# Kernel optimization log

Hardware: AMD Instinct MI355X
Metric: run time of the kernel (lower is better)

The kernel has to match this reference:

```python
import jax, jax.numpy as jnp
import numpy as np

N_NODES = 100000


def gcn_layer(x, W, b, src, dst, n):
    # PyG GCNConv: h = x @ W; add self loops; norm = d^-1/2[src]*d^-1/2[dst];
    # out = scatter_add(norm * h[src] -> dst) + b
    h = x @ W  # [N, F_out]
    # append self loops
    loop = jnp.arange(n, dtype=src.dtype)
    s = jnp.concatenate([src, loop])
    d = jnp.concatenate([dst, loop])
    deg = jax.ops.segment_sum(jnp.ones_like(d, dtype=h.dtype), d, num_segments=n)
    dinv = jnp.where(deg > 0, jax.lax.rsqrt(deg), 0.0)
    norm = dinv[s] * dinv[d]  # [E+N]
    msg = h[s] * norm[:, None]  # gather + scale
    out = jax.ops.segment_sum(msg, d, num_segments=n)  # scatter-add
    return out + b


def setup_inputs() -> dict:
    key = jax.random.key(0)
    k1, k2, k3, k4 = jax.random.split(key, 4)
    din, dh = 64, 64
    x = jax.random.normal(k1, (N_NODES, din), dtype=jnp.float32)
    edge_index = jax.random.randint(k2, (2, 1600000), 0, N_NODES, dtype=jnp.int64)
    s1 = 1.0 / np.sqrt(din)
    s2 = 1.0 / np.sqrt(dh)
    W1 = jax.random.uniform(k3, (din, dh), dtype=jnp.float32, minval=-s1, maxval=s1)
    W2 = jax.random.uniform(k4, (dh, dh), dtype=jnp.float32, minval=-s2, maxval=s2)
    b1 = jnp.zeros((dh,), dtype=jnp.float32)
    b2 = jnp.zeros((dh,), dtype=jnp.float32)
    return {"x": x, "edge_index": edge_index, "W1": W1, "b1": b1, "W2": W2, "b2": b2}


def reference(x, edge_index, W1, b1, W2, b2):
    src, dst = edge_index[0], edge_index[1]
    n = x.shape[0]
    h = jax.nn.relu(gcn_layer(x, W1, b1, src, dst, n))
    h = jax.nn.relu(gcn_layer(h, W2, b2, src, dst, n))
    return h
```

## Files before the change

kernel.cpp:

```cpp
#include <hip/hip_runtime.h>
#include <hip/hip_bf16.h>

using bf16s = __hip_bfloat16;
typedef __bf16 bf16x8 __attribute__((ext_vector_type(8)));
typedef float f32x4 __attribute__((ext_vector_type(4)));

constexpr int MS_TILE = 2048;
constexpr int BSH = 7;
constexpr int BN = 128;
constexpr int NBUCK_MAX = 1024;
constexpr int SLAB_CAP = 2560;
constexpr int CSR_CAP = 3584;

__device__ inline float uasf(unsigned u) { return __uint_as_float(u); }

__device__ inline unsigned pk2(float x, float y) {
    unsigned ux = __float_as_uint(x), uy = __float_as_uint(y);
    ux = (ux + 0x7fffu + ((ux >> 16) & 1u)) >> 16;
    uy = (uy + 0x7fffu + ((uy >> 16) & 1u)) & 0xffff0000u;
    return (ux & 0xffffu) | uy;
}

__global__ __launch_bounds__(256) void multisplit(const int* __restrict__ src,
                                                  const int* __restrict__ dst,
                                                  int* __restrict__ gcur,
                                                  int* __restrict__ part, int E) {
    __shared__ int cnt[NBUCK_MAX];
    __shared__ int off[NBUCK_MAX];
    __shared__ int gbase[NBUCK_MAX];
    __shared__ int img[MS_TILE];
    __shared__ int tgt[MS_TILE];
    int tid = threadIdx.x;
    for (int tbase = blockIdx.x * MS_TILE; tbase < E; tbase += gridDim.x * MS_TILE) {
        int m = min(MS_TILE, E - tbase);
        for (int i = tid; i < NBUCK_MAX; i += 256) cnt[i] = 0;
        __syncthreads();
        int pk[8], bk[8], rk[8];
        int nloc = 0;
        int j0 = tid * 8;
        if (j0 + 8 <= m) {
            int4 s0 = *(const int4*)(src + tbase + j0);
            int4 s1 = *(const int4*)(src + tbase + j0 + 4);
            int4 d0 = *(const int4*)(dst + tbase + j0);
            int4 d1 = *(const int4*)(dst + tbase + j0 + 4);
            int ss[8] = {s0.x, s0.y, s0.z, s0.w, s1.x, s1.y, s1.z, s1.w};
            int dd[8] = {d0.x, d0.y, d0.z, d0.w, d1.x, d1.y, d1.z, d1.w};
#pragma unroll
            for (int k = 0; k < 8; k++) {
                int b = dd[k] >> BSH;
                pk[k] = (ss[k] << BSH) | (dd[k] & (BN - 1));
                bk[k] = b;
                rk[k] = atomicAdd(&cnt[b], 1);
            }
            nloc = 8;
        } else {
            for (int j = j0; j < m; j++) {
                int s = src[tbase + j], d = dst[tbase + j];
                int b = d >> BSH;
                pk[nloc] = (s << BSH) | (d & (BN - 1));
                bk[nloc] = b;
                rk[nloc] = atomicAdd(&cnt[b], 1);
                nloc++;
            }
        }
        __syncthreads();
        if (tid < 64) {
            int base = tid * 16;
            int vals[16];
            int s0 = 0;
#pragma unroll
            for (int j = 0; j < 16; j++) { vals[j] = cnt[base + j]; s0 += vals[j]; }
            int sc = s0;
#pragma unroll
            for (int o = 1; o < 64; o <<= 1) {
                int u = __shfl_up(sc, o);
                if (tid >= o) sc += u;
            }
            int ex = sc - s0;
#pragma unroll
            for (int j = 0; j < 16; j++) { off[base + j] = ex; ex += vals[j]; }
        }
        __syncthreads();
        for (int b = tid; b < NBUCK_MAX; b += 256) {
            int c = cnt[b];
            if (c) {
                int st = atomicAdd(&gcur[b], c);
                if (st > SLAB_CAP - c) st = SLAB_CAP - c;
                gbase[b] = b * SLAB_CAP + st;
            }
        }
        __syncthreads();
        for (int i = 0; i < nloc; i++) {
            int p = off[bk[i]] + rk[i];
            img[p] = pk[i];
            tgt[p] = gbase[bk[i]] + rk[i];
        }
        __syncthreads();
        for (int j = tid; j < m; j += 256) part[tgt[j]] = img[j];
        __syncthreads();
    }
}

__global__ __launch_bounds__(256) void bucket_place(const int* __restrict__ gcur,
                                                    const int* __restrict__ part,
                                                    int2* __restrict__ rinfo,
                                                    int* __restrict__ csr,
                                                    float* __restrict__ dinv, int n) {
    __shared__ int cnt[BN];
    __shared__ int cur[BN];
    __shared__ int wtot[4];
    __shared__ int img[CSR_CAP];
    int b = blockIdx.x;
    int tid = threadIdx.x;
    int node0 = b << BSH;
    int m = min(gcur[b], SLAB_CAP);
    const int* slab = part + b * SLAB_CAP;
    if (tid < BN) cnt[tid] = 0;
    __syncthreads();
    for (int j = tid; j < m; j += 256) atomicAdd(&cnt[slab[j] & (BN - 1)], 1);
    __syncthreads();
    int deg = (tid < BN) ? cnt[tid] : 0;
    int pdeg = (deg + 7) & ~7;
    int lane = tid & 63, wv = tid >> 6;
    int sc = pdeg;
#pragma unroll
    for (int o = 1; o < 64; o <<= 1) {
        int u = __shfl_up(sc, o);
        if (lane >= o) sc += u;
    }
    if (lane == 63) wtot[wv] = sc;
    __syncthreads();
    int mpad = wtot[0] + wtot[1];
    if (tid < BN) {
        int ex = sc - pdeg + (wv ? wtot[0] : 0);
        cur[tid] = ex;
        int node = node0 + tid;
        if (node < n) {
            rinfo[node] = make_int2(b * CSR_CAP + ex, pdeg);
            dinv[node] = rsqrtf((float)(deg + 1));
        }
    }
    __syncthreads();
    int sent = n << 5;
    for (int j = tid; j < mpad; j += 256) img[j] = sent;
    __syncthreads();
    for (int j = tid; j < m; j += 256) {
        int pkv = slab[j];
        int p = atomicAdd(&cur[pkv & (BN - 1)], 1);
        img[p] = (pkv >> BSH) << 5;
    }
    __syncthreads();
    int* dp = csr + b * CSR_CAP;
    for (int j = tid; j < mpad; j += 256) dp[j] = img[j];
}

template <bool AF32>
__global__ __launch_bounds__(256) void gemm64(const void* __restrict__ A_,
                                              const float* __restrict__ W,
                                              const float* __restrict__ dinv,
                                              bf16s* __restrict__ out, int nrows) {
    int lane = threadIdx.x & 63;
    int wid = (blockIdx.x * blockDim.x + threadIdx.x) >> 6;
    int nwaves = (gridDim.x * blockDim.x) >> 6;
    int r = lane & 15;
    int q = lane >> 4;
    int kb = q * 8;

    if (wid == 0) out[(size_t)nrows * 64 + lane] = __float2bfloat16(0.f);

    bf16x8 bfrag[4][2];
#pragma unroll
    for (int t = 0; t < 4; t++) {
#pragma unroll
        for (int h = 0; h < 2; h++) {
            bf16x8 bb;
            int ncol = t * 16 + r;
            int k0 = h * 32 + kb;
#pragma unroll
            for (int j = 0; j < 8; j++) bb[j] = (__bf16)W[(k0 + j) * 64 + ncol];
            bfrag[t][h] = bb;
        }
    }

    int ntiles = nrows >> 4;
    for (int tile = wid; tile < ntiles; tile += nwaves) {
        bf16x8 a0, a1;
        if (AF32) {
            const float* ap = (const float*)A_ + (size_t)(tile * 16 + r) * 64 + kb;
            f32x4 v0 = *reinterpret_cast<const f32x4*>(ap);
            f32x4 v1 = *reinterpret_cast<const f32x4*>(ap + 4);
            f32x4 v2 = *reinterpret_cast<const f32x4*>(ap + 32);
            f32x4 v3 = *reinterpret_cast<const f32x4*>(ap + 36);
#pragma unroll
            for (int j = 0; j < 4; j++) {
                a0[j] = (__bf16)v0[j]; a0[4 + j] = (__bf16)v1[j];
                a1[j] = (__bf16)v2[j]; a1[4 + j] = (__bf16)v3[j];
            }
        } else {
            const __bf16* ap = (const __bf16*)A_ + (size_t)(tile * 16 + r) * 64 + kb;
            a0 = *reinterpret_cast<const bf16x8*>(ap);
            a1 = *reinterpret_cast<const bf16x8*>(ap + 32);
        }
        f32x4 c[4];
#pragma unroll
        for (int t = 0; t < 4; t++) {
            f32x4 acc = {0.f, 0.f, 0.f, 0.f};
            acc = __builtin_amdgcn_mfma_f32_16x16x32_bf16(a0, bfrag[t][0], acc, 0, 0, 0);
            acc = __builtin_amdgcn_mfma_f32_16x16x32_bf16(a1, bfrag[t][1], acc, 0, 0, 0);
            c[t] = acc;
        }
        float dr[4];
#pragma unroll
        for (int g = 0; g < 4; g++) dr[g] = dinv[tile * 16 + q * 4 + g];
#pragma unroll
        for (int t = 0; t < 4; t++) {
#pragma unroll
            for (int g = 0; g < 4; g++) {
                int row = tile * 16 + q * 4 + g;
                out[(size_t)row * 64 + t * 16 + r] = __float2bfloat16(c[t][g] * dr[g]);
            }
        }
    }
}

template <bool OUTF32>
__global__ __launch_bounds__(256) void aggregate(const unsigned* __restrict__ t32,
                                                 const float* __restrict__ dinv,
                                                 const int2* __restrict__ rinfo,
                                                 const int* __restrict__ csr,
                                                 const float* __restrict__ bias,
                                                 void* __restrict__ out_, int n) {
    int gid = blockIdx.x * blockDim.x + threadIdx.x;
    int v = gid >> 4;
    if (v >= n) return;
    int c = gid & 15;
    int2 ri = rinfo[v];
    uint2 sw = *(const uint2*)(t32 + (size_t)v * 32 + 2 * c);
    float a0 = uasf(sw.x << 16), a1 = uasf(sw.x & 0xffff0000u);
    float a2 = uasf(sw.y << 16), a3 = uasf(sw.y & 0xffff0000u);
    const int* cp = csr + ri.x;
    for (int j = 0; j < ri.y; j += 8) {
        int4 e0 = *(const int4*)(cp + j);
        int4 e1 = *(const int4*)(cp + j + 4);
        int idx[8] = {e0.x, e0.y, e0.z, e0.w, e1.x, e1.y, e1.z, e1.w};
        uint2 g[8];
#pragma unroll
        for (int k = 0; k < 8; k++)
            g[k] = *(const uint2*)(t32 + (size_t)idx[k] + 2 * c);
#pragma unroll
        for (int k = 0; k < 8; k++) {
            a0 += uasf(g[k].x << 16);
            a1 += uasf(g[k].x & 0xffff0000u);
            a2 += uasf(g[k].y << 16);
            a3 += uasf(g[k].y & 0xffff0000u);
        }
    }
    float dv = dinv[v];
    f32x4 bb = ((const f32x4*)bias)[c];
    float o0 = fmaxf(fmaf(dv, a0, bb[0]), 0.f);
    float o1 = fmaxf(fmaf(dv, a1, bb[1]), 0.f);
    float o2 = fmaxf(fmaf(dv, a2, bb[2]), 0.f);
    float o3 = fmaxf(fmaf(dv, a3, bb[3]), 0.f);
    if (OUTF32) {
        f32x4 o4 = {o0, o1, o2, o3};
        ((f32x4*)out_)[(size_t)v * 16 + c] = o4;
    } else {
        uint2 o2u;
        o2u.x = pk2(o0, o1);
        o2u.y = pk2(o2, o3);
        ((uint2*)out_)[(size_t)v * 16 + c] = o2u;
    }
}

extern "C" void kernel_launch(void* const* d_in, const int* in_sizes, int n_in,
                              void* d_out, int out_size, void* d_ws, size_t ws_size,
                              hipStream_t stream) {
    const float* x  = (const float*)d_in[0];
    const int*   ei = (const int*)d_in[1];
    const float* W1 = (const float*)d_in[2];
    const float* b1 = (const float*)d_in[3];
    const float* W2 = (const float*)d_in[4];
    const float* b2 = (const float*)d_in[5];
    float* out = (float*)d_out;

    int n = in_sizes[0] / 64;
    int E = in_sizes[1] / 2;
    const int* src = ei;
    const int* dst = ei + E;
    int nbuck = (n + BN - 1) >> BSH;

    char* w = (char*)d_ws;
    auto alloc = [&](size_t bytes) -> void* {
        void* p = (void*)w;
        w += (bytes + 255) & ~(size_t)255;
        return p;
    };
    int*   gcur   = (int*)alloc(NBUCK_MAX * 4);
    int2*  rinfo  = (int2*)alloc((size_t)n * 8);
    int*   csr    = (int*)alloc((size_t)nbuck * CSR_CAP * 4);
    float* dinv   = (float*)alloc((size_t)n * 4);
    size_t slab_bytes = (size_t)nbuck * SLAB_CAP * 4;
    size_t tbuf_bytes = (size_t)(n + 16) * 64 * 2;
    char*  ovl    = (char*)alloc(slab_bytes > tbuf_bytes ? slab_bytes : tbuf_bytes);
    int*   part   = (int*)ovl;
    bf16s* tbuf   = (bf16s*)ovl;
    bf16s* h1     = (bf16s*)alloc((size_t)(n + 16) * 64 * 2);

    hipMemsetAsync(gcur, 0, NBUCK_MAX * 4, stream);

    int ntiles = (E + MS_TILE - 1) / MS_TILE;
    multisplit<<<ntiles, 256, 0, stream>>>(src, dst, gcur, part, E);
    bucket_place<<<nbuck, 256, 0, stream>>>(gcur, part, rinfo, csr, dinv, n);

    int agrid = (n * 16 + 255) / 256;
    gemm64<true><<<256, 256, 0, stream>>>(x, W1, dinv, tbuf, n);
    aggregate<false><<<agrid, 256, 0, stream>>>((const unsigned*)tbuf, dinv, rinfo, csr, b1, h1, n);
    gemm64<false><<<256, 256, 0, stream>>>(h1, W2, dinv, tbuf, n);
    aggregate<true><<<agrid, 256, 0, stream>>>((const unsigned*)tbuf, dinv, rinfo, csr, b2, out, n);
}
```

Before: 205.9 us.

## Use 256-node buckets, larger multisplit tiles, and two nodes per aggregate thread

Bucket width is doubled to 256 nodes, so there are fewer buckets and the slab and CSR capacities grow with them. The multisplit kernel now handles one 4096-edge tile per block with 16 edges per thread and no grid-stride loop. The aggregate kernel gives each 16-lane group two destination nodes and interleaves their gathers, which raises memory-level parallelism per thread and halves the grid. This risks load imbalance when the two nodes have different degrees, plus higher register use and more LDS in bucket_place.

```diff
diff --git a/kernel.cpp b/kernel.cpp
--- a/kernel.cpp
+++ b/kernel.cpp
@@ -5,12 +5,12 @@
 typedef __bf16 bf16x8 __attribute__((ext_vector_type(8)));
 typedef float f32x4 __attribute__((ext_vector_type(4)));
 
-constexpr int MS_TILE = 2048;
-constexpr int BSH = 7;
-constexpr int BN = 128;
-constexpr int NBUCK_MAX = 1024;
-constexpr int SLAB_CAP = 2560;
-constexpr int CSR_CAP = 3584;
+constexpr int MS_TILE = 4096;
+constexpr int BSH = 8;
+constexpr int BN = 256;
+constexpr int NBUCK = 512;
+constexpr int SLAB_CAP = 5120;
+constexpr int CSR_CAP = 7168;
 
 __device__ inline float uasf(unsigned u) { return __uint_as_float(u); }
 
@@ -25,80 +25,80 @@
                                                   const int* __restrict__ dst,
                                                   int* __restrict__ gcur,
                                                   int* __restrict__ part, int E) {
-    __shared__ int cnt[NBUCK_MAX];
-    __shared__ int off[NBUCK_MAX];
-    __shared__ int gbase[NBUCK_MAX];
+    __shared__ int cnt[NBUCK];
+    __shared__ int off[NBUCK];
+    __shared__ int gbase[NBUCK];
     __shared__ int img[MS_TILE];
     __shared__ int tgt[MS_TILE];
     int tid = threadIdx.x;
-    for (int tbase = blockIdx.x * MS_TILE; tbase < E; tbase += gridDim.x * MS_TILE) {
-        int m = min(MS_TILE, E - tbase);
-        for (int i = tid; i < NBUCK_MAX; i += 256) cnt[i] = 0;
-        __syncthreads();
-        int pk[8], bk[8], rk[8];
-        int nloc = 0;
-        int j0 = tid * 8;
-        if (j0 + 8 <= m) {
-            int4 s0 = *(const int4*)(src + tbase + j0);
-            int4 s1 = *(const int4*)(src + tbase + j0 + 4);
-            int4 d0 = *(const int4*)(dst + tbase + j0);
-            int4 d1 = *(const int4*)(dst + tbase + j0 + 4);
-            int ss[8] = {s0.x, s0.y, s0.z, s0.w, s1.x, s1.y, s1.z, s1.w};
-            int dd[8] = {d0.x, d0.y, d0.z, d0.w, d1.x, d1.y, d1.z, d1.w};
-#pragma unroll
-            for (int k = 0; k < 8; k++) {
+    int tbase = blockIdx.x * MS_TILE;
+    int m = min(MS_TILE, E - tbase);
+    for (int i = tid; i < NBUCK; i += 256) cnt[i] = 0;
+    __syncthreads();
+    int pk[16], bk[16], rk[16];
+    int nloc = 0;
+    int j0 = tid * 16;
+    if (j0 + 16 <= m) {
+#pragma unroll
+        for (int h = 0; h < 4; h++) {
+            int4 s4 = *(const int4*)(src + tbase + j0 + 4 * h);
+            int4 d4 = *(const int4*)(dst + tbase + j0 + 4 * h);
+            int ss[4] = {s4.x, s4.y, s4.z, s4.w};
+            int dd[4] = {d4.x, d4.y, d4.z, d4.w};
+#pragma unroll
+            for (int k = 0; k < 4; k++) {
+                int i = 4 * h + k;
                 int b = dd[k] >> BSH;
-                pk[k] = (ss[k] << BSH) | (dd[k] & (BN - 1));
-                bk[k] = b;
-                rk[k] = atomicAdd(&cnt[b], 1);
-            }
-            nloc = 8;
-        } else {
-            for (int j = j0; j < m; j++) {
-                int s = src[tbase + j], d = dst[tbase + j];
-                int b = d >> BSH;
-                pk[nloc] = (s << BSH) | (d & (BN - 1));
-                bk[nloc] = b;
-                rk[nloc] = atomicAdd(&cnt[b], 1);
-                nloc++;
-            }
-        }
-        __syncthreads();
-        if (tid < 64) {
-            int base = tid * 16;
-            int vals[16];
-            int s0 = 0;
-#pragma unroll
-            for (int j = 0; j < 16; j++) { vals[j] = cnt[base + j]; s0 += vals[j]; }
-            int sc = s0;
-#pragma unroll
-            for (int o = 1; o < 64; o <<= 1) {
-                int u = __shfl_up(sc, o);
-                if (tid >= o) sc += u;
-            }
-            int ex = sc - s0;
-#pragma unroll
-            for (int j = 0; j < 16; j++) { off[base + j] = ex; ex += vals[j]; }
-        }
-        __syncthreads();
-        for (int b = tid; b < NBUCK_MAX; b += 256) {
-            int c = cnt[b];
-            if (c) {
-                int st = atomicAdd(&gcur[b], c);
-                if (st > SLAB_CAP - c) st = SLAB_CAP - c;
-                gbase[b] = b * SLAB_CAP + st;
-            }
-        }
-        __syncthreads();
-        for (int i = 0; i < nloc; i++) {
-            int p = off[bk[i]] + rk[i];
-            img[p] = pk[i];
-            tgt[p] = gbase[bk[i]] + rk[i];
-        }
-        __syncthreads();
-        for (int j = tid; j < m; j += 256) part[tgt[j]] = img[j];
-        __syncthreads();
-    }
+                pk[i] = (ss[k] << BSH) | (dd[k] & (BN - 1));
+                bk[i] = b;
+                rk[i] = atomicAdd(&cnt[b], 1);
+            }
+        }
+        nloc = 16;
+    } else {
+        for (int j = j0; j < m; j++) {
+            int s = src[tbase + j], d = dst[tbase + j];
+            int b = d >> BSH;
+            pk[nloc] = (s << BSH) | (d & (BN - 1));
+            bk[nloc] = b;
+            rk[nloc] = atomicAdd(&cnt[b], 1);
+            nloc++;
+        }
+    }
+    __syncthreads();
+    if (tid < 64) {
+        int base = tid * 8;
+        int vals[8];
+        int s0 = 0;
+#pragma unroll
+        for (int j = 0; j < 8; j++) { vals[j] = cnt[base + j]; s0 += vals[j]; }
+        int sc = s0;
+#pragma unroll
+        for (int o = 1; o < 64; o <<= 1) {
+            int u = __shfl_up(sc, o);
+            if (tid >= o) sc += u;
+        }
+        int ex = sc - s0;
+#pragma unroll
+        for (int j = 0; j < 8; j++) { off[base + j] = ex; ex += vals[j]; }
+    }
+    __syncthreads();
+    for (int b = tid; b < NBUCK; b += 256) {
+        int c = cnt[b];
+        if (c) {
+            int st = atomicAdd(&gcur[b], c);
+            if (st > SLAB_CAP - c) st = SLAB_CAP - c;
+            gbase[b] = b * SLAB_CAP + st;
+        }
+    }
+    __syncthreads();
+    for (int i = 0; i < nloc; i++) {
+        int p = off[bk[i]] + rk[i];
+        img[p] = pk[i];
+        tgt[p] = gbase[bk[i]] + rk[i];
+    }
+    __syncthreads();
+    for (int j = tid; j < m; j += 256) part[tgt[j]] = img[j];
 }
 
 __global__ __launch_bounds__(256) void bucket_place(const int* __restrict__ gcur,
@@ -115,11 +115,11 @@
     int node0 = b << BSH;
     int m = min(gcur[b], SLAB_CAP);
     const int* slab = part + b * SLAB_CAP;
-    if (tid < BN) cnt[tid] = 0;
+    cnt[tid] = 0;
     __syncthreads();
     for (int j = tid; j < m; j += 256) atomicAdd(&cnt[slab[j] & (BN - 1)], 1);
     __syncthreads();
-    int deg = (tid < BN) ? cnt[tid] : 0;
+    int deg = cnt[tid];
     int pdeg = (deg + 7) & ~7;
     int lane = tid & 63, wv = tid >> 6;
     int sc = pdeg;
@@ -130,15 +130,16 @@
     }
     if (lane == 63) wtot[wv] = sc;
     __syncthreads();
-    int mpad = wtot[0] + wtot[1];
-    if (tid < BN) {
-        int ex = sc - pdeg + (wv ? wtot[0] : 0);
-        cur[tid] = ex;
-        int node = node0 + tid;
-        if (node < n) {
-            rinfo[node] = make_int2(b * CSR_CAP + ex, pdeg);
-            dinv[node] = rsqrtf((float)(deg + 1));
-        }
+    int wbase = 0;
+#pragma unroll
+    for (int k = 0; k < 4; k++) wbase += (k < wv) ? wtot[k] : 0;
+    int mpad = wtot[0] + wtot[1] + wtot[2] + wtot[3];
+    int ex = sc - pdeg + wbase;
+    cur[tid] = ex;
+    int node = node0 + tid;
+    if (node < n) {
+        rinfo[node] = make_int2(b * CSR_CAP + ex, pdeg);
+        dinv[node] = rsqrtf((float)(deg + 1));
     }
     __syncthreads();
     int sent = n << 5;
@@ -231,44 +232,93 @@
                                                  const float* __restrict__ bias,
                                                  void* __restrict__ out_, int n) {
     int gid = blockIdx.x * blockDim.x + threadIdx.x;
-    int v = gid >> 4;
-    if (v >= n) return;
+    int qw = gid >> 4;
+    int v0 = qw * 2, v1 = v0 + 1;
+    if (v0 >= n) return;
+    bool has1 = v1 < n;
     int c = gid & 15;
-    int2 ri = rinfo[v];
-    uint2 sw = *(const uint2*)(t32 + (size_t)v * 32 + 2 * c);
-    float a0 = uasf(sw.x << 16), a1 = uasf(sw.x & 0xffff0000u);
-    float a2 = uasf(sw.y << 16), a3 = uasf(sw.y & 0xffff0000u);
-    const int* cp = csr + ri.x;
-    for (int j = 0; j < ri.y; j += 8) {
-        int4 e0 = *(const int4*)(cp + j);
-        int4 e1 = *(const int4*)(cp + j + 4);
-        int idx[8] = {e0.x, e0.y, e0.z, e0.w, e1.x, e1.y, e1.z, e1.w};
-        uint2 g[8];
-#pragma unroll
-        for (int k = 0; k < 8; k++)
-            g[k] = *(const uint2*)(t32 + (size_t)idx[k] + 2 * c);
-#pragma unroll
-        for (int k = 0; k < 8; k++) {
-            a0 += uasf(g[k].x << 16);
-            a1 += uasf(g[k].x & 0xffff0000u);
-            a2 += uasf(g[k].y << 16);
-            a3 += uasf(g[k].y & 0xffff0000u);
-        }
-    }
-    float dv = dinv[v];
+    int2 r0 = rinfo[v0];
+    int2 r1 = has1 ? rinfo[v1] : make_int2(0, 0);
+    uint2 s0 = *(const uint2*)(t32 + (size_t)v0 * 32 + 2 * c);
+    uint2 s1 = has1 ? *(const uint2*)(t32 + (size_t)v1 * 32 + 2 * c) : make_uint2(0, 0);
+    float a00 = uasf(s0.x << 16), a01 = uasf(s0.x & 0xffff0000u);
+    float a02 = uasf(s0.y << 16), a03 = uasf(s0.y & 0xffff0000u);
+    float a10 = uasf(s1.x << 16), a11 = uasf(s1.x & 0xffff0000u);
+    float a12 = uasf(s1.y << 16), a13 = uasf(s1.y & 0xffff0000u);
+    const int* cp0 = csr + r0.x;
+    const int* cp1 = csr + r1.x;
+    int j0 = 0, j1 = 0;
+    while (j0 < r0.y || j1 < r1.y) {
+        bool g0 = j0 < r0.y, g1 = j1 < r1.y;
+        int idx0[8], idx1[8];
+        uint2 ga[8], gb[8];
+        if (g0) {
+            int4 e0 = *(const int4*)(cp0 + j0);
+            int4 e1 = *(const int4*)(cp0 + j0 + 4);
+            idx0[0]=e0.x; idx0[1]=e0.y; idx0[2]=e0.z; idx0[3]=e0.w;
+            idx0[4]=e1.x; idx0[5]=e1.y; idx0[6]=e1.z; idx0[7]=e1.w;
+#pragma unroll
+            for (int k = 0; k < 8; k++)
+                ga[k] = *(const uint2*)(t32 + (size_t)idx0[k] + 2 * c);
+        }
+        if (g1) {
+            int4 e0 = *(const int4*)(cp1 + j1);
+            int4 e1 = *(const int4*)(cp1 + j1 + 4);
+            idx1[0]=e0.x; idx1[1]=e0.y; idx1[2]=e0.z; idx1[3]=e0.w;
+            idx1[4]=e1.x; idx1[5]=e1.y; idx1[6]=e1.z; idx1[7]=e1.w;
+#pragma unroll
+            for (int k = 0; k < 8; k++)
+                gb[k] = *(const uint2*)(t32 + (size_t)idx1[k] + 2 * c);
+        }
+        if (g0) {
+#pragma unroll
+            for (int k = 0; k < 8; k++) {
+                a00 += uasf(ga[k].x << 16);
+                a01 += uasf(ga[k].x & 0xffff0000u);
+                a02 += uasf(ga[k].y << 16);
+                a03 += uasf(ga[k].y & 0xffff0000u);
+            }
+            j0 += 8;
+        }
+        if (g1) {
+#pragma unroll
+            for (int k = 0; k < 8; k++) {
+                a10 += uasf(gb[k].x << 16);
+                a11 += uasf(gb[k].x & 0xffff0000u);
+                a12 += uasf(gb[k].y << 16);
+                a13 += uasf(gb[k].y & 0xffff0000u);
+            }
+            j1 += 8;
+        }
+    }
     f32x4 bb = ((const f32x4*)bias)[c];
-    float o0 = fmaxf(fmaf(dv, a0, bb[0]), 0.f);
-    float o1 = fmaxf(fmaf(dv, a1, bb[1]), 0.f);
-    float o2 = fmaxf(fmaf(dv, a2, bb[2]), 0.f);
-    float o3 = fmaxf(fmaf(dv, a3, bb[3]), 0.f);
-    if (OUTF32) {
-        f32x4 o4 = {o0, o1, o2, o3};
-        ((f32x4*)out_)[(size_t)v * 16 + c] = o4;
-    } else {
-        uint2 o2u;
-        o2u.x = pk2(o0, o1);
-        o2u.y = pk2(o2, o3);
-        ((uint2*)out_)[(size_t)v * 16 + c] = o2u;
+    {
+        float dv = dinv[v0];
+        float o0 = fmaxf(fmaf(dv, a00, bb[0]), 0.f);
+        float o1 = fmaxf(fmaf(dv, a01, bb[1]), 0.f);
+        float o2 = fmaxf(fmaf(dv, a02, bb[2]), 0.f);
+        float o3 = fmaxf(fmaf(dv, a03, bb[3]), 0.f);
+        if (OUTF32) {
+            f32x4 o4 = {o0, o1, o2, o3};
+            ((f32x4*)out_)[(size_t)v0 * 16 + c] = o4;
+        } else {
+            uint2 ou; ou.x = pk2(o0, o1); ou.y = pk2(o2, o3);
+            ((uint2*)out_)[(size_t)v0 * 16 + c] = ou;
+        }
+    }
+    if (has1) {
+        float dv = dinv[v1];
+        float o0 = fmaxf(fmaf(dv, a10, bb[0]), 0.f);
+        float o1 = fmaxf(fmaf(dv, a11, bb[1]), 0.f);
+        float o2 = fmaxf(fmaf(dv, a12, bb[2]), 0.f);
+        float o3 = fmaxf(fmaf(dv, a13, bb[3]), 0.f);
+        if (OUTF32) {
+            f32x4 o4 = {o0, o1, o2, o3};
+            ((f32x4*)out_)[(size_t)v1 * 16 + c] = o4;
+        } else {
+            uint2 ou; ou.x = pk2(o0, o1); ou.y = pk2(o2, o3);
+            ((uint2*)out_)[(size_t)v1 * 16 + c] = ou;
+        }
     }
 }
 
@@ -295,7 +345,7 @@
         w += (bytes + 255) & ~(size_t)255;
         return p;
     };
-    int*   gcur   = (int*)alloc(NBUCK_MAX * 4);
+    int*   gcur   = (int*)alloc(NBUCK * 4);
     int2*  rinfo  = (int2*)alloc((size_t)n * 8);
     int*   csr    = (int*)alloc((size_t)nbuck * CSR_CAP * 4);
     float* dinv   = (float*)alloc((size_t)n * 4);
@@ -306,13 +356,13 @@
     bf16s* tbuf   = (bf16s*)ovl;
     bf16s* h1     = (bf16s*)alloc((size_t)(n + 16) * 64 * 2);
 
-    hipMemsetAsync(gcur, 0, NBUCK_MAX * 4, stream);
+    hipMemsetAsync(gcur, 0, NBUCK * 4, stream);
 
     int ntiles = (E + MS_TILE - 1) / MS_TILE;
     multisplit<<<ntiles, 256, 0, stream>>>(src, dst, gcur, part, E);
     bucket_place<<<nbuck, 256, 0, stream>>>(gcur, part, rinfo, csr, dinv, n);
 
-    int agrid = (n * 16 + 255) / 256;
+    int agrid = (n * 8 + 255) / 256;
     gemm64<true><<<256, 256, 0, stream>>>(x, W1, dinv, tbuf, n);
     aggregate<false><<<agrid, 256, 0, stream>>>((const unsigned*)tbuf, dinv, rinfo, csr, b1, h1, n);
     gemm64<false><<<256, 256, 0, stream>>>(h1, W2, dinv, tbuf, n);
```

Result: faster. 201.9 us (-2.0%).
